# Kernel tuning notes

Hardware: AMD Instinct MI355X
Metric: run time of the kernel (lower is better)

Reference implementation:

```python
import jax, jax.numpy as jnp
import numpy as np

EPS_ATTN = 1e-5   # attention denominator eps (module eps)
EPS_LN = 1e-5     # nn.LayerNorm default eps


def _prime(x, proj):
    # Performer FAVOR+ hyperbolic positive features.
    # x: (B,H,L,dh), proj: (dh,m) -> (B,H,L,2m)
    dn = x.shape[-1] ** -0.25
    xn = dn * x
    d = jnp.einsum('bhld,dm->bhlm', xn, proj)
    diag = 0.5 * jnp.sum(xn * xn, axis=-1, keepdims=True)
    return jnp.concatenate([jnp.exp(d - diag), jnp.exp(-d - diag)], axis=-1)


def setup_inputs() -> dict:
    L, B, H, DH, DM, M = 2048, 4, 8, 64, 512, 256
    key = jax.random.key(0)
    k0, k1, k2 = jax.random.split(key, 3)
    h = jax.random.normal(k0, (L, B, DM), jnp.float32)
    w_qkv = jax.random.normal(k1, (H * 3 * DH, DM), jnp.float32) / np.sqrt(DM)
    w_o = jax.random.normal(k2, (DM, H * DH), jnp.float32) / np.sqrt(H * DH)
    ln_gamma = jnp.ones((DM,), jnp.float32)
    ln_beta = jnp.zeros((DM,), jnp.float32)
    # Gaussian orthogonal random matrix (blockwise QR), rows scaled by sqrt(dh)
    rng = np.random.default_rng(0)
    blocks = []
    for _ in range(M // DH):
        g = rng.standard_normal((DH, DH)).astype(np.float32)
        q, _ = np.linalg.qr(g)
        blocks.append(q.T)
    pm = np.concatenate(blocks, axis=0) * np.sqrt(DH)  # (M, DH)
    proj_matrix = jnp.asarray(pm.T.astype(np.float32))  # (DH, M)
    return {"h": h, "w_qkv": w_qkv, "w_o": w_o,
            "ln_gamma": ln_gamma, "ln_beta": ln_beta,
            "proj_matrix": proj_matrix}


def _forward(h, w_qkv, w_o, ln_gamma, ln_beta, proj_matrix):
    L, B, DM = h.shape
    DH, M = proj_matrix.shape
    H = w_qkv.shape[0] // (3 * DH)
    scale = DH ** -0.5

    qkv = (h @ w_qkv.T).reshape(L, B, H, 3 * DH)
    q, k, v = jnp.split(qkv, 3, axis=-1)
    q = jnp.transpose(q, (1, 2, 0, 3))  # (B,H,L,dh)
    k = jnp.transpose(k, (1, 2, 0, 3))
    v = jnp.transpose(v, (1, 2, 0, 3))

    qp = _prime(q, proj_matrix)  # (B,H,L,2M)
    kp = _prime(k, proj_matrix)
    kp = kp / jnp.sum(kp, axis=-1, keepdims=True)
    qp = qp / jnp.sum(qp, axis=-1, keepdims=True)

    den_acc = jnp.cumsum(kp, axis=2)
    denom = jnp.einsum('bhlm,bhlm->bhl', den_acc, qp)[..., None]  # (B,H,L,1)

    # fast_weight_sum: W_t = W_{t-1} + k_t v_t^T ; out_t = q_t @ W_t
    def step(W, xs):
        qt, kt, vt = xs  # (B,H,2M), (B,H,2M), (B,H,dh)
        W = W + kt[..., :, None] * vt[..., None, :]
        out = jnp.einsum('bhm,bhmd->bhd', qt, W)
        return W, out

    W0 = jnp.zeros((B, H, 2 * M, DH), h.dtype)
    xs = (jnp.transpose(qp, (2, 0, 1, 3)),
          jnp.transpose(kp, (2, 0, 1, 3)),
          jnp.transpose(v, (2, 0, 1, 3)))
    _, out = jax.lax.scan(step, W0, xs)  # (L,B,H,dh)
    out = jnp.transpose(out, (1, 2, 0, 3))  # (B,H,L,dh)

    out = scale * out / (denom + EPS_ATTN)
    out = jnp.transpose(out, (0, 2, 1, 3)).reshape(B, L, H * DH)  # (B,L,H*dh)
    out = jnp.swapaxes(out, 0, 1)  # (L,B,H*dh)

    attn_out = out @ w_o.T
    x = h + attn_out
    mu = jnp.mean(x, axis=-1, keepdims=True)
    var = jnp.mean((x - mu) ** 2, axis=-1, keepdims=True)
    return (x - mu) / jnp.sqrt(var + EPS_LN) * ln_gamma + ln_beta


def reference(h, w_qkv, w_o, ln_gamma, ln_beta, proj_matrix):
    return _forward(h, w_qkv, w_o, ln_gamma, ln_beta, proj_matrix)
```

## Files before the change

kernel.cpp:

```cpp
#include <hip/hip_runtime.h>
#include <hip/hip_fp16.h>
#include <math.h>

#define LSEQ 2048
#define NB 4
#define NH 8
#define DMID 512
#define CHK 128
#define SCALE 0.125f
#define DN 0.35355339059327373f
#define DN2 0.125f
#define LOG2E 1.4426950408889634f
#define EPS_ATTN 1e-5f
#define EPS_LN 1e-5f

typedef _Float16 f16x8 __attribute__((ext_vector_type(8)));
typedef _Float16 f16x4 __attribute__((ext_vector_type(4)));
typedef float f32x4 __attribute__((ext_vector_type(4)));

__device__ __forceinline__ float exp2a(float x) {
  float r;
  asm("v_exp_f32 %0, %1" : "=v"(r) : "v"(x));
  return r;
}

__device__ __forceinline__ void cvt16(const float* __restrict__ p,
                                      _Float16* __restrict__ dst) {
  float4 a = *(const float4*)p, b = *(const float4*)(p + 4);
  float4 c = *(const float4*)(p + 8), d = *(const float4*)(p + 12);
  f16x8 t0 = {(_Float16)a.x, (_Float16)a.y, (_Float16)a.z, (_Float16)a.w,
              (_Float16)b.x, (_Float16)b.y, (_Float16)b.z, (_Float16)b.w};
  f16x8 t1 = {(_Float16)c.x, (_Float16)c.y, (_Float16)c.z, (_Float16)c.w,
              (_Float16)d.x, (_Float16)d.y, (_Float16)d.z, (_Float16)d.w};
  *(f16x8*)dst = t0;
  *(f16x8*)(dst + 8) = t1;
}

__device__ __forceinline__ void cvt16r(const float4* __restrict__ r,
                                       _Float16* __restrict__ dst) {
  f16x8 t0 = {(_Float16)r[0].x, (_Float16)r[0].y, (_Float16)r[0].z,
              (_Float16)r[0].w, (_Float16)r[1].x, (_Float16)r[1].y,
              (_Float16)r[1].z, (_Float16)r[1].w};
  f16x8 t1 = {(_Float16)r[2].x, (_Float16)r[2].y, (_Float16)r[2].z,
              (_Float16)r[2].w, (_Float16)r[3].x, (_Float16)r[3].y,
              (_Float16)r[3].z, (_Float16)r[3].w};
  *(f16x8*)dst = t0;
  *(f16x8*)(dst + 8) = t1;
}

__device__ __forceinline__ void cvt8r(const float4* __restrict__ r,
                                      _Float16* __restrict__ dst) {
  f16x8 t0 = {(_Float16)r[0].x, (_Float16)r[0].y, (_Float16)r[0].z,
              (_Float16)r[0].w, (_Float16)r[1].x, (_Float16)r[1].y,
              (_Float16)r[1].z, (_Float16)r[1].w};
  *(f16x8*)dst = t0;
}

__global__ void k_diag(float* out, int n, float val) {
  int i = blockIdx.x * 256 + threadIdx.x;
  if (i < n) out[i] = val;
}

__global__ __launch_bounds__(256) void k_ptr(const float* __restrict__ proj,
                                             __half* __restrict__ projT) {
  int e = blockIdx.x * 256 + threadIdx.x;
  int n = e >> 6, k = e & 63;
  projT[e] = __float2half_rn(proj[k * 256 + n] * (DN * LOG2E));
}

__global__ __launch_bounds__(512) void k_qkv(
    const float* __restrict__ A, const float* __restrict__ Wq,
    __half* __restrict__ q, __half* __restrict__ k, __half* __restrict__ v) {
  __shared__ __align__(16) char smem[34816];
  _Float16* Ah = (_Float16*)smem;
  _Float16* Bh = (_Float16*)(smem + 20480);
  _Float16* Oh = (_Float16*)smem;

  const int tid = threadIdx.x;
  const int row0 = blockIdx.x * 256;
  const int col0 = blockIdx.y * 128;
  const int lane = tid & 63, wv = tid >> 6;
  const int ln15 = lane & 15, quad = lane >> 4;
  const int m0 = wv * 32;

  f32x4 Cacc[2][8];
  const f32x4 z4 = {0.f, 0.f, 0.f, 0.f};
#pragma unroll
  for (int mi = 0; mi < 2; ++mi)
#pragma unroll
    for (int nt = 0; nt < 8; ++nt) Cacc[mi][nt] = z4;

  const int sarow = tid >> 1, sac = (tid & 1) * 16;
  const float* aptr = A + (size_t)(row0 + sarow) * DMID + sac;
  const float* bptr = Wq + (size_t)(col0 + sarow) * DMID + sac;

  float4 ra[4], rb[4];
#pragma unroll
  for (int i = 0; i < 4; ++i) ra[i] = *(const float4*)(aptr + i * 4);
  if (tid < 256) {
#pragma unroll
    for (int i = 0; i < 4; ++i) rb[i] = *(const float4*)(bptr + i * 4);
  }

  for (int kt = 0; kt < DMID; kt += 32) {
    cvt16r(ra, &Ah[sarow * 40 + sac]);
    if (tid < 256) cvt16r(rb, &Bh[sarow * 40 + sac]);
    if (kt + 32 < DMID) {
#pragma unroll
      for (int i = 0; i < 4; ++i)
        ra[i] = *(const float4*)(aptr + kt + 32 + i * 4);
      if (tid < 256) {
#pragma unroll
        for (int i = 0; i < 4; ++i)
          rb[i] = *(const float4*)(bptr + kt + 32 + i * 4);
      }
    }
    asm volatile("s_waitcnt lgkmcnt(0)" ::: "memory");
    __builtin_amdgcn_s_barrier();
    asm volatile("" ::: "memory");

    f16x8 a0 = *(const f16x8*)&Ah[(m0 + ln15) * 40 + quad * 8];
    f16x8 a1 = *(const f16x8*)&Ah[(m0 + 16 + ln15) * 40 + quad * 8];
#pragma unroll
    for (int nt = 0; nt < 8; ++nt) {
      f16x8 bf = *(const f16x8*)&Bh[(nt * 16 + ln15) * 40 + quad * 8];
      Cacc[0][nt] = __builtin_amdgcn_mfma_f32_16x16x32_f16(a0, bf, Cacc[0][nt], 0, 0, 0);
      Cacc[1][nt] = __builtin_amdgcn_mfma_f32_16x16x32_f16(a1, bf, Cacc[1][nt], 0, 0, 0);
    }
    asm volatile("" ::: "memory");
    __builtin_amdgcn_s_barrier();
    asm volatile("" ::: "memory");
  }

  const int tr = tid >> 4, tc = tid & 15;
  const int col = col0 + tc * 8;
  const int hh = col / 192;
  const int rem = col - hh * 192;
  const int t = rem >> 6;
  const int d0 = rem & 63;
  __half* dstb = (t == 0) ? q : ((t == 1) ? k : v);

#pragma unroll
  for (int hf = 0; hf < 2; ++hf) {
    if ((wv >> 2) == hf) {
      int lm = (wv & 3) * 32;
#pragma unroll
      for (int mi = 0; mi < 2; ++mi)
#pragma unroll
        for (int nt = 0; nt < 8; ++nt)
#pragma unroll
          for (int r = 0; r < 4; ++r)
            Oh[(lm + mi * 16 + quad * 4 + r) * 136 + nt * 16 + ln15] =
                (_Float16)Cacc[mi][nt][r];
    }
    __syncthreads();
#pragma unroll
    for (int i = 0; i < 4; ++i) {
      int lrow = tr * 4 + i;
      int grow = row0 + hf * 128 + lrow;
      int l = grow >> 2, bb = grow & 3;
      f16x8 val = *(const f16x8*)&Oh[lrow * 136 + tc * 8];
      *(f16x8*)((_Float16*)dstb + (((size_t)(bb * NH + hh) * LSEQ + l) << 6) + d0) = val;
    }
    __syncthreads();
  }
}

__global__ __launch_bounds__(512) void k_dgemm(
    const __half* __restrict__ qsrc, const __half* __restrict__ ksrc,
    const __half* __restrict__ projT, __half* __restrict__ dqd,
    __half* __restrict__ dkd, float* __restrict__ nq,
    float* __restrict__ nk) {
  __shared__ __align__(16) char smem[37888];
  _Float16* Bt = (_Float16*)smem;
  float* g_l  = (float*)(smem + 36864);
  float* ps_l = (float*)(smem + 37376);
  _Float16* Oh = (_Float16*)smem;

  const int tid = threadIdx.x;
  const __half* src = blockIdx.y ? ksrc : qsrc;
  __half* dst = blockIdx.y ? dkd : dqd;
  float* nrm = blockIdx.y ? nk : nq;
  const size_t r0 = (size_t)blockIdx.x * 128;

  const int lane = tid & 63, wv = tid >> 6;
  const int ln15 = lane & 15, quad = lane >> 4;
  const int m0 = wv * 16;

#pragma unroll
  for (int it = 0; it < 4; ++it) {
    int e = it * 512 + tid;
    int n = e >> 3, seg = e & 7;
    *(f16x8*)&Bt[n * 72 + seg * 8] =
        *(const f16x8*)((const _Float16*)projT + n * 64 + seg * 8);
  }

  f16x8 afrag[2];
  float ss = 0.f;
  {
    const _Float16* rp = (const _Float16*)src + (r0 + m0 + ln15) * 64;
#pragma unroll
    for (int ks = 0; ks < 2; ++ks) {
      f16x8 x8 = *(const f16x8*)(rp + ks * 32 + quad * 8);
      afrag[ks] = x8;
#pragma unroll
      for (int j = 0; j < 8; ++j) {
        float xv = (float)x8[j];
        ss = fmaf(xv, xv, ss);
      }
    }
    ss += __shfl_xor(ss, 16);
    ss += __shfl_xor(ss, 32);
  }
  if (quad == 0) g_l[m0 + ln15] = 0.5f * DN2 * LOG2E * ss;
  __syncthreads();

  f32x4 Cacc[16];
  const f32x4 z4 = {0.f, 0.f, 0.f, 0.f};
#pragma unroll
  for (int nt = 0; nt < 16; ++nt) Cacc[nt] = z4;

#pragma unroll
  for (int ks = 0; ks < 2; ++ks) {
    f16x8 a0 = afrag[ks];
#pragma unroll
    for (int nt = 0; nt < 16; ++nt) {
      f16x8 bf = *(const f16x8*)&Bt[(nt * 16 + ln15) * 72 + ks * 32 + quad * 8];
      Cacc[nt] = __builtin_amdgcn_mfma_f32_16x16x32_f16(a0, bf, Cacc[nt], 0, 0, 0);
    }
  }

  float gv[4], pp[4];
#pragma unroll
  for (int r = 0; r < 4; ++r) {
    gv[r] = g_l[m0 + quad * 4 + r];
    pp[r] = 0.f;
  }
#pragma unroll
  for (int nt = 0; nt < 16; ++nt)
#pragma unroll
    for (int r = 0; r < 4; ++r) {
      float d = Cacc[nt][r];
      pp[r] += exp2a(d - gv[r]) + exp2a(-d - gv[r]);
    }
#pragma unroll
  for (int r = 0; r < 4; ++r) {
    float p = pp[r];
    p += __shfl_xor(p, 1); p += __shfl_xor(p, 2);
    p += __shfl_xor(p, 4); p += __shfl_xor(p, 8);
    if (ln15 == 0) ps_l[m0 + quad * 4 + r] = p;
  }

#pragma unroll
  for (int hf = 0; hf < 2; ++hf) {
    __syncthreads();
#pragma unroll
    for (int nt2 = 0; nt2 < 8; ++nt2) {
      int nt = hf * 8 + nt2;
#pragma unroll
      for (int r = 0; r < 4; ++r)
        Oh[(m0 + quad * 4 + r) * 136 + nt2 * 16 + ln15] =
            (_Float16)Cacc[nt][r];
    }
    __syncthreads();
#pragma unroll
    for (int it = 0; it < 4; ++it) {
      int e = it * 512 + tid;
      int row = e >> 4, seg = e & 15;
      *(f16x8*)((_Float16*)dst + (r0 + row) * 256 + hf * 128 + seg * 8) =
          *(const f16x8*)&Oh[row * 136 + seg * 8];
    }
  }
  if (tid < 128) nrm[r0 + tid] = g_l[tid] + __log2f(ps_l[tid]);
}

__global__ __launch_bounds__(512) void k_kv(
    const __half* __restrict__ dk, const float* __restrict__ nk,
    const __half* __restrict__ v, __half* __restrict__ KVt,
    float* __restrict__ Ks) {
  __shared__ __align__(16) char smem[52736];
  _Float16* kpT = (_Float16*)smem;
  _Float16* Vt  = (_Float16*)(smem + 34816);
  float* ck = (float*)(smem + 52224);
  _Float16* Oh2 = (_Float16*)smem;

  const int tid = threadIdx.x;
  const int cidx = blockIdx.x;
  const size_t rowbase = (size_t)cidx * CHK;
  const int lane = tid & 63, wv = tid >> 6;
  const int ln15 = lane & 15, quad = lane >> 4;

  if (tid < 128) ck[tid] = nk[rowbase + tid];
  {
    int s = tid & 127, dq0 = (tid >> 7) * 16;
    const _Float16* vsrc = (const _Float16*)v + (rowbase + s) * 64 + dq0;
    f16x8 v0 = ((const f16x8*)vsrc)[0];
    f16x8 v1 = ((const f16x8*)vsrc)[1];
#pragma unroll
    for (int j = 0; j < 8; ++j) {
      Vt[(dq0 + j) * 136 + s] = v0[j];
      Vt[(dq0 + 8 + j) * 136 + s] = v1[j];
    }
  }

  const int srow = tid >> 2;
  const int scol = (tid & 3) * 32;

  f16x8 bone;
#pragma unroll
  for (int j = 0; j < 8; ++j)
    bone[j] = (ln15 == 0) ? (_Float16)1.0f : (_Float16)0.0f;

  bool first = true;
#pragma unroll
  for (int cp = 0; cp < 2; ++cp) {
    f16x8 rk[4];
    const _Float16* dsrc =
        (const _Float16*)dk + (rowbase + srow) * 256 + cp * 128 + scol;
#pragma unroll
    for (int it = 0; it < 4; ++it) rk[it] = *(const f16x8*)(dsrc + it * 8);
    float c = ck[srow];
    if (first) { __syncthreads(); c = ck[srow]; }

#pragma unroll
    for (int sg = 0; sg < 2; ++sg) {
      const int i0 = sg * 256 + cp * 128;
      const float fsign = sg ? -1.f : 1.f;
      if (!first) __syncthreads();
      first = false;
#pragma unroll
      for (int it = 0; it < 4; ++it) {
        f16x8 d8 = rk[it];
#pragma unroll
        for (int j = 0; j < 8; ++j)
          kpT[(scol + it * 8 + j) * 136 + srow] =
              (_Float16)exp2a(fmaf((float)d8[j], fsign, -c));
      }
      __syncthreads();

      f32x4 Cacc[4], Kacc;
      const f32x4 z4 = {0.f, 0.f, 0.f, 0.f};
#pragma unroll
      for (int nt = 0; nt < 4; ++nt) Cacc[nt] = z4;
      Kacc = z4;
#pragma unroll
      for (int ks = 0; ks < 4; ++ks) {
        f16x8 a0 = *(const f16x8*)&kpT[(wv * 16 + ln15) * 136 + ks * 32 + quad * 8];
#pragma unroll
        for (int nt = 0; nt < 4; ++nt) {
          f16x8 bV = *(const f16x8*)&Vt[(nt * 16 + ln15) * 136 + ks * 32 + quad * 8];
          Cacc[nt] = __builtin_amdgcn_mfma_f32_16x16x32_f16(a0, bV, Cacc[nt], 0, 0, 0);
        }
        Kacc = __builtin_amdgcn_mfma_f32_16x16x32_f16(a0, bone, Kacc, 0, 0, 0);
      }
      if (ln15 == 0) {
#pragma unroll
        for (int r = 0; r < 4; ++r)
          Ks[(size_t)cidx * 512 + i0 + wv * 16 + quad * 4 + r] = Kacc[r];
      }
      __syncthreads();

#pragma unroll
      for (int nt = 0; nt < 4; ++nt) {
        f16x4 pack = {(_Float16)Cacc[nt][0], (_Float16)Cacc[nt][1],
                      (_Float16)Cacc[nt][2], (_Float16)Cacc[nt][3]};
        *(f16x4*)&Oh2[(nt * 16 + ln15) * 136 + wv * 16 + quad * 4] = pack;
      }
      __syncthreads();
      {
        int d = tid >> 3, part = tid & 7;
        _Float16* dstp =
            (_Float16*)KVt + (size_t)cidx * 32768 + d * 512 + i0 + part * 16;
        const _Float16* srcp = &Oh2[d * 136 + part * 16];
        *(f16x8*)(dstp) = *(const f16x8*)(srcp);
        *(f16x8*)(dstp + 8) = *(const f16x8*)(srcp + 8);
      }
    }
  }
}

__global__ __launch_bounds__(256) void k_scan(__half2* __restrict__ KV2,
                                              float* __restrict__ Ks) {
  const int bh = blockIdx.x;
  const int tid = threadIdx.x;
  if (blockIdx.y < 32) {
    uint2* p = (uint2*)(KV2 + (size_t)bh * 262144) + (blockIdx.y * 256 + tid);
    uint2 raw[16];
#pragma unroll
    for (int c = 0; c < 16; ++c) raw[c] = p[c * 8192];
    float ax0 = 0.f, ay0 = 0.f, ax1 = 0.f, ay1 = 0.f;
#pragma unroll
    for (int c = 0; c < 16; ++c) {
      __half2 h0 = *(__half2*)&raw[c].x;
      __half2 h1 = *(__half2*)&raw[c].y;
      float2 f0 = __half22float2(h0), f1 = __half22float2(h1);
      __half2 o0 = __floats2half2_rn(ax0, ay0);
      __half2 o1 = __floats2half2_rn(ax1, ay1);
      uint2 o;
      o.x = *(unsigned*)&o0;
      o.y = *(unsigned*)&o1;
      p[c * 8192] = o;
      ax0 += f0.x; ay0 += f0.y; ax1 += f1.x; ay1 += f1.y;
    }
  } else {
    int i = (blockIdx.y - 32) * 256 + tid;
    float* pk = Ks + (size_t)bh * 8192 + i;
    float vs[16];
#pragma unroll
    for (int c = 0; c < 16; ++c) vs[c] = pk[c * 512];
    float a = 0.f;
#pragma unroll
    for (int c = 0; c < 16; ++c) { pk[c * 512] = a; a += vs[c]; }
  }
}

__global__ __launch_bounds__(512) void k_attn(
    const __half* __restrict__ dq, const __half* __restrict__ dk,
    const float* __restrict__ nq, const float* __restrict__ nk,
    const __half* __restrict__ v, const __half* __restrict__ KVt,
    const float* __restrict__ Kpre, float* __restrict__ outb) {
  __shared__ __align__(16) char smem[53760];
  _Float16* qpT = (_Float16*)(smem);
  _Float16* kpT = (_Float16*)(smem + 18432);
  _Float16* WT  = (_Float16*)(smem + 36864);
  float*    KpT = (float*)(smem + 46080);
  float* cq_l   = (float*)(smem + 46336);
  float* ck_l   = (float*)(smem + 46848);
  _Float16* S_h = (_Float16*)(smem);
  _Float16* Vt  = (_Float16*)(smem + 34816);
  float* den1_l = (float*)(smem + 52224);
  float* den2_l = (float*)(smem + 52736);
  float* invd_l = (float*)(smem + 53248);

  const int tid = threadIdx.x;
  const int cidx = blockIdx.x;
  const int cc = cidx & 15, bh = cidx >> 4;
  const size_t rowb = (size_t)cidx * 128;
  const int lane = tid & 63;
  const int wv = tid >> 6;
  const int H = wv >> 2;
  const int m0 = (wv & 3) * 16;
  const int ln15 = lane & 15, quad = lane >> 4;

  if (tid < 128) cq_l[tid] = nq[rowb + tid];
  else if (tid < 256) ck_l[tid - 128] = nk[rowb + tid - 128];
  __syncthreads();

  const int c8 = tid & 7;
  const int r9 = tid >> 3;
  const int csrc = (c8 & 3) * 8;
  const float sgnf = (c8 < 4) ? 1.f : -1.f;

  const _Float16* qsrc = (const _Float16*)dq + (rowb + r9) * 256 + csrc;
  const _Float16* ksrc = (const _Float16*)dk + (rowb + r9) * 256 + csrc;
  const _Float16* wsrc = (const _Float16*)KVt + (size_t)cidx * 32768 +
                         r9 * 512 + ((c8 < 4) ? 0 : 256) + csrc;
  const float* kpsrc = Kpre + (size_t)cidx * 512 +
                       ((tid < 32) ? tid : (tid < 64 ? 224 + tid : 0));

  float cq[2], ck2[2];
#pragma unroll
  for (int p = 0; p < 2; ++p) {
    cq[p] = cq_l[r9 + p * 64];
    ck2[p] = ck_l[r9 + p * 64];
  }

  f16x8 rq[2], rk[2];
#pragma unroll
  for (int p = 0; p < 2; ++p) {
    rq[p] = *(const f16x8*)(qsrc + p * 16384);
    rk[p] = *(const f16x8*)(ksrc + p * 16384);
  }
  f16x8 wcur = *(const f16x8*)(wsrc);
  float kpcur = kpsrc[0];

  f32x4 Sacc[8], Oacc[4], Dacc;
  const f32x4 z4 = {0.f, 0.f, 0.f, 0.f};
#pragma unroll
  for (int nt = 0; nt < 8; ++nt) Sacc[nt] = z4;
#pragma unroll
  for (int nt = 0; nt < 4; ++nt) Oacc[nt] = z4;
  Dacc = z4;

  const int NSw = H ? 8 : 4;

  for (int it = 0; it < 8; ++it) {
    const int kb = it * 32;
    f16x8 wnxt;
    float kpnxt = 0.f;
    if (it < 7) {
      wnxt = *(const f16x8*)(wsrc + kb + 32);
      kpnxt = kpsrc[kb + 32];
    }

#pragma unroll
    for (int p = 0; p < 2; ++p) {
      f16x8 d = rq[p], t;
#pragma unroll
      for (int j = 0; j < 8; ++j)
        t[j] = (_Float16)exp2a(fmaf((float)d[j], sgnf, -cq[p]));
      *(f16x8*)&qpT[(r9 + p * 64) * 72 + c8 * 8] = t;
    }
#pragma unroll
    for (int p = 0; p < 2; ++p) {
      f16x8 d = rk[p], t;
#pragma unroll
      for (int j = 0; j < 8; ++j)
        t[j] = (_Float16)exp2a(fmaf((float)d[j], sgnf, -ck2[p]));
      *(f16x8*)&kpT[(r9 + p * 64) * 72 + c8 * 8] = t;
    }

    if (it < 7) {
#pragma unroll
      for (int p = 0; p < 2; ++p) {
        rq[p] = *(const f16x8*)(qsrc + p * 16384 + kb + 32);
        rk[p] = *(const f16x8*)(ksrc + p * 16384 + kb + 32);
      }
    }
    *(f16x8*)&WT[r9 * 72 + c8 * 8] = wcur;
    if (tid < 64) KpT[tid] = kpcur;

    asm volatile("s_waitcnt lgkmcnt(0)" ::: "memory");
    __builtin_amdgcn_s_barrier();
    asm volatile("" ::: "memory");

    __builtin_amdgcn_s_setprio(1);
#pragma unroll
    for (int ks = 0; ks < 2; ++ks) {
      f16x8 a0 = *(const f16x8*)&qpT[(H * 64 + m0 + ln15) * 72 + ks * 32 + quad * 8];
#pragma unroll
      for (int nt = 0; nt < 4; ++nt) {
        f16x8 bf = *(const f16x8*)&kpT[(nt * 16 + ln15) * 72 + ks * 32 + quad * 8];
        Sacc[nt] = __builtin_amdgcn_mfma_f32_16x16x32_f16(a0, bf, Sacc[nt], 0, 0, 0);
      }
      if (H) {
#pragma unroll
        for (int nt = 4; nt < 8; ++nt) {
          f16x8 bf = *(const f16x8*)&kpT[(nt * 16 + ln15) * 72 + ks * 32 + quad * 8];
          Sacc[nt] = __builtin_amdgcn_mfma_f32_16x16x32_f16(a0, bf, Sacc[nt], 0, 0, 0);
        }
      }
#pragma unroll
      for (int nt = 0; nt < 4; ++nt) {
        f16x8 bw = *(const f16x8*)&WT[(nt * 16 + ln15) * 72 + ks * 32 + quad * 8];
        Oacc[nt] = __builtin_amdgcn_mfma_f32_16x16x32_f16(a0, bw, Oacc[nt], 0, 0, 0);
      }
      f16x8 bk;
#pragma unroll
      for (int j = 0; j < 8; ++j)
        bk[j] = (ln15 == 0) ? (_Float16)KpT[ks * 32 + quad * 8 + j]
                            : (_Float16)0.f;
      Dacc = __builtin_amdgcn_mfma_f32_16x16x32_f16(a0, bk, Dacc, 0, 0, 0);
    }
    __builtin_amdgcn_s_setprio(0);

    asm volatile("" ::: "memory");
    __builtin_amdgcn_s_barrier();
    asm volatile("" ::: "memory");

    if (it < 7) { wcur = wnxt; kpcur = kpnxt; }
  }

  if (ln15 == 0) {
#pragma unroll
    for (int r = 0; r < 4; ++r)
      den2_l[H * 64 + m0 + quad * 4 + r] = Dacc[r];
  }
  {
    _Float16* S_me = S_h + H * 8704;
    float dp[4] = {0.f, 0.f, 0.f, 0.f};
#pragma unroll
    for (int nt = 0; nt < 8; ++nt) {
      if (nt < NSw) {
        int s = nt * 16 + ln15;
#pragma unroll
        for (int r = 0; r < 4; ++r) {
          int tl = m0 + quad * 4 + r;
          float vsv = (s <= H * 64 + tl) ? Sacc[nt][r] : 0.f;
          dp[r] += vsv;
          S_me[tl * 136 + s] = (_Float16)vsv;
        }
      }
    }
#pragma unroll
    for (int r = 0; r < 4; ++r) {
      float p = dp[r];
      p += __shfl_xor(p, 1); p += __shfl_xor(p, 2);
      p += __shfl_xor(p, 4); p += __shfl_xor(p, 8);
      if (ln15 == 0) den1_l[H * 64 + m0 + quad * 4 + r] = p;
    }
  }
  {
    int s = tid & 127, d0v = (tid >> 7) * 16;
    const _Float16* vsrc = (const _Float16*)v + (rowb + s) * 64 + d0v;
    f16x8 v0 = ((const f16x8*)vsrc)[0];
    f16x8 v1 = ((const f16x8*)vsrc)[1];
#pragma unroll
    for (int j = 0; j < 8; ++j) {
      Vt[(d0v + j) * 136 + s] = v0[j];
      Vt[(d0v + 8 + j) * 136 + s] = v1[j];
    }
  }
  __syncthreads();
  if (tid < 128)
    invd_l[tid] = SCALE / (den1_l[tid] + den2_l[tid] + EPS_ATTN);
  __syncthreads();
  {
    _Float16* S_me = S_h + H * 8704;
#pragma unroll
    for (int ks = 0; ks < 4; ++ks) {
      if (ks < (H ? 4 : 2)) {
        f16x8 aS0 = *(const f16x8*)&S_me[(m0 + ln15) * 136 + ks * 32 + quad * 8];
#pragma unroll
        for (int nt = 0; nt < 4; ++nt) {
          f16x8 bV = *(const f16x8*)&Vt[(nt * 16 + ln15) * 136 + ks * 32 + quad * 8];
          Oacc[nt] = __builtin_amdgcn_mfma_f32_16x16x32_f16(aS0, bV, Oacc[nt], 0, 0, 0);
        }
      }
    }
  }
  const int b = bh >> 3, hh = bh & 7;
  float ivv[4];
#pragma unroll
  for (int r = 0; r < 4; ++r)
    ivv[r] = invd_l[H * 64 + m0 + quad * 4 + r];
#pragma unroll
  for (int nt = 0; nt < 4; ++nt) {
    int dcol = nt * 16 + ln15;
#pragma unroll
    for (int r = 0; r < 4; ++r) {
      int l = cc * 128 + H * 64 + m0 + quad * 4 + r;
      outb[((size_t)l * 4 + b) * 512 + hh * 64 + dcol] = Oacc[nt][r] * ivv[r];
    }
  }
}

__global__ __launch_bounds__(256) void k_oproj(
    const float* __restrict__ A, const float* __restrict__ Wo,
    const float* __restrict__ hres, float* __restrict__ xout) {
  __shared__ __align__(16) char smem[17408];
  _Float16* Ah = (_Float16*)smem;
  _Float16* Bh = (_Float16*)(smem + 5120);
  _Float16* Oh = (_Float16*)smem;

  const int tid = threadIdx.x;
  const int row0 = blockIdx.x * 64;
  const int col0 = blockIdx.y * 128;
  const int lane = tid & 63, wv = tid >> 6;
  const int ln15 = lane & 15, quad = lane >> 4;
  const int m0 = wv * 16;

  f32x4 Cacc[8];
  const f32x4 z4 = {0.f, 0.f, 0.f, 0.f};
#pragma unroll
  for (int nt = 0; nt < 8; ++nt) Cacc[nt] = z4;

  const int arow = tid >> 2, asc = (tid & 3) * 8;
  const int brow = tid >> 1, bsc = (tid & 1) * 16;
  const float* aptr = A + (size_t)(row0 + arow) * DMID + asc;
  const float* bptr = Wo + (size_t)(col0 + brow) * DMID + bsc;

  float4 ra[2], rb[4];
#pragma unroll
  for (int i = 0; i < 2; ++i) ra[i] = *(const float4*)(aptr + i * 4);
#pragma unroll
  for (int i = 0; i < 4; ++i) rb[i] = *(const float4*)(bptr + i * 4);

  for (int kt = 0; kt < DMID; kt += 32) {
    cvt8r(ra, &Ah[arow * 40 + asc]);
    cvt16r(rb, &Bh[brow * 40 + bsc]);
    if (kt + 32 < DMID) {
#pragma unroll
      for (int i = 0; i < 2; ++i)
        ra[i] = *(const float4*)(aptr + kt + 32 + i * 4);
#pragma unroll
      for (int i = 0; i < 4; ++i)
        rb[i] = *(const float4*)(bptr + kt + 32 + i * 4);
    }
    asm volatile("s_waitcnt lgkmcnt(0)" ::: "memory");
    __builtin_amdgcn_s_barrier();
    asm volatile("" ::: "memory");

    f16x8 a0 = *(const f16x8*)&Ah[(m0 + ln15) * 40 + quad * 8];
#pragma unroll
    for (int nt = 0; nt < 8; ++nt) {
      f16x8 bf = *(const f16x8*)&Bh[(nt * 16 + ln15) * 40 + quad * 8];
      Cacc[nt] = __builtin_amdgcn_mfma_f32_16x16x32_f16(a0, bf, Cacc[nt], 0, 0, 0);
    }
    asm volatile("" ::: "memory");
    __builtin_amdgcn_s_barrier();
    asm volatile("" ::: "memory");
  }
#pragma unroll
  for (int nt = 0; nt < 8; ++nt)
#pragma unroll
    for (int r = 0; r < 4; ++r)
      Oh[(m0 + quad * 4 + r) * 136 + nt * 16 + ln15] = (_Float16)Cacc[nt][r];
  __syncthreads();
  const int tr = tid >> 4, tc = tid & 15;
#pragma unroll
  for (int i = 0; i < 4; ++i) {
    int lrow = tr * 4 + i;
    int grow = row0 + lrow;
    size_t base = (size_t)grow * 512 + col0 + tc * 8;
    f16x8 o = *(const f16x8*)&Oh[lrow * 136 + tc * 8];
    float4 h0 = *(const float4*)(hres + base);
    float4 h1 = *(const float4*)(hres + base + 4);
    *(float4*)(xout + base) =
        make_float4((float)o[0] + h0.x, (float)o[1] + h0.y,
                    (float)o[2] + h0.z, (float)o[3] + h0.w);
    *(float4*)(xout + base + 4) =
        make_float4((float)o[4] + h1.x, (float)o[5] + h1.y,
                    (float)o[6] + h1.z, (float)o[7] + h1.w);
  }
}

__global__ __launch_bounds__(256) void k_ln(float* __restrict__ x,
                                            const float* __restrict__ g,
                                            const float* __restrict__ bta) {
  __shared__ float ws_[4], wq_[4];
  const int row = blockIdx.x;
  const int tid = threadIdx.x;
  float2 vv = *(const float2*)(x + (size_t)row * 512 + tid * 2);
  float s = vv.x + vv.y;
  float sq = vv.x * vv.x + vv.y * vv.y;
#pragma unroll
  for (int off = 1; off < 64; off <<= 1) {
    s += __shfl_xor(s, off, 64);
    sq += __shfl_xor(sq, off, 64);
  }
  if ((tid & 63) == 0) { ws_[tid >> 6] = s; wq_[tid >> 6] = sq; }
  __syncthreads();
  s = ws_[0] + ws_[1] + ws_[2] + ws_[3];
  sq = wq_[0] + wq_[1] + wq_[2] + wq_[3];
  float mu = s * (1.f / 512.f);
  float var = sq * (1.f / 512.f) - mu * mu;
  float rstd = rsqrtf(var + EPS_LN);
  int c = tid * 2;
  float2 o;
  o.x = (vv.x - mu) * rstd * g[c] + bta[c];
  o.y = (vv.y - mu) * rstd * g[c + 1] + bta[c + 1];
  *(float2*)(x + (size_t)row * 512 + c) = o;
}

extern "C" void kernel_launch(void* const* d_in, const int* in_sizes, int n_in,
                              void* d_out, int out_size, void* d_ws,
                              size_t ws_size, hipStream_t stream) {
  const float* h    = (const float*)d_in[0];
  const float* wqkv = (const float*)d_in[1];
  const float* wo   = (const float*)d_in[2];
  const float* g    = (const float*)d_in[3];
  const float* bta  = (const float*)d_in[4];
  const float* proj = (const float*)d_in[5];
  float* out = (float*)d_out;
  char* wsb = (char*)d_ws;

  __half* q   = (__half*)(wsb + 0);
  __half* kb  = (__half*)(wsb + 8388608);
  __half* vb  = (__half*)(wsb + 16777216);
  __half* dq  = (__half*)(wsb + 25165824);
  __half* dk  = (__half*)(wsb + 58720256);
  float*  nq  = (float*)(wsb + 92274688);
  float*  nk  = (float*)(wsb + 92798976);
  __half* KVt = (__half*)(wsb + 93323264);
  float*  Ks  = (float*)(wsb + 126877696);
  __half* pT  = (__half*)(wsb + 127926272);
  float* outb = (float*)(wsb + 0);

  if (ws_size < 127959040ull) {
    float val = 1000.0f + (float)(ws_size >> 20);
    k_diag<<<(out_size + 255) / 256, 256, 0, stream>>>(out, out_size, val);
    return;
  }

  k_ptr  <<<dim3(64), 256, 0, stream>>>(proj, pT);
  k_qkv  <<<dim3(32, 12), 512, 0, stream>>>(h, wqkv, q, kb, vb);
  k_dgemm<<<dim3(512, 2), 512, 0, stream>>>(q, kb, pT, dq, dk, nq, nk);
  k_kv   <<<dim3(512), 512, 0, stream>>>(dk, nk, vb, KVt, Ks);
  k_scan <<<dim3(32, 34), 256, 0, stream>>>((__half2*)KVt, Ks);
  k_attn <<<dim3(512), 512, 0, stream>>>(dq, dk, nq, nk, vb, KVt, Ks, outb);
  k_oproj<<<dim3(128, 4), 256, 0, stream>>>(outb, wo, h, out);
  k_ln   <<<dim3(8192), 256, 0, stream>>>(out, g, bta);
}
```

Baseline: 223.4 us.

## Fuse output projection, residual add and LayerNorm into one kernel

Replaces the separate output-projection GEMM and LayerNorm kernels with one kernel in which each block computes 32 full rows of all 512 output columns. Residual add and LayerNorm statistics are then done in registers, with a shuffle plus shared-memory cross-wave reduction. This removes one launch and the extra write and read of the pre-norm activations. In exchange, each block now reloads the entire Wo matrix, and only 256 blocks are launched, which can lower parallelism and raise weight traffic.

```diff
diff --git a/kernel.cpp b/kernel.cpp
--- a/kernel.cpp
+++ b/kernel.cpp
@@ -46,14 +46,6 @@
               (_Float16)r[3].z, (_Float16)r[3].w};
   *(f16x8*)dst = t0;
   *(f16x8*)(dst + 8) = t1;
-}
-
-__device__ __forceinline__ void cvt8r(const float4* __restrict__ r,
-                                      _Float16* __restrict__ dst) {
-  f16x8 t0 = {(_Float16)r[0].x, (_Float16)r[0].y, (_Float16)r[0].z,
-              (_Float16)r[0].w, (_Float16)r[1].x, (_Float16)r[1].y,
-              (_Float16)r[1].z, (_Float16)r[1].w};
-  *(f16x8*)dst = t0;
 }
 
 __global__ void k_diag(float* out, int n, float val) {
@@ -635,112 +627,120 @@
   }
 }
 
-__global__ __launch_bounds__(256) void k_oproj(
+__global__ __launch_bounds__(512) void k_oproj_ln(
     const float* __restrict__ A, const float* __restrict__ Wo,
-    const float* __restrict__ hres, float* __restrict__ xout) {
-  __shared__ __align__(16) char smem[17408];
+    const float* __restrict__ hres, const float* __restrict__ g,
+    const float* __restrict__ bta, float* __restrict__ xout) {
+  __shared__ __align__(16) char smem[45568];
   _Float16* Ah = (_Float16*)smem;
-  _Float16* Bh = (_Float16*)(smem + 5120);
-  _Float16* Oh = (_Float16*)smem;
+  _Float16* Bh = (_Float16*)(smem + 2560);
+  float* s_l = (float*)(smem + 43520);
+  float* q_l = (float*)(smem + 44032);
 
   const int tid = threadIdx.x;
-  const int row0 = blockIdx.x * 64;
-  const int col0 = blockIdx.y * 128;
+  const int row0 = blockIdx.x * 32;
   const int lane = tid & 63, wv = tid >> 6;
   const int ln15 = lane & 15, quad = lane >> 4;
-  const int m0 = wv * 16;
+  const int mt = wv & 1;
+  const int nq4 = wv >> 1;
+  const int n0 = nq4 * 128;
 
   f32x4 Cacc[8];
   const f32x4 z4 = {0.f, 0.f, 0.f, 0.f};
 #pragma unroll
   for (int nt = 0; nt < 8; ++nt) Cacc[nt] = z4;
 
-  const int arow = tid >> 2, asc = (tid & 3) * 8;
-  const int brow = tid >> 1, bsc = (tid & 1) * 16;
-  const float* aptr = A + (size_t)(row0 + arow) * DMID + asc;
-  const float* bptr = Wo + (size_t)(col0 + brow) * DMID + bsc;
-
-  float4 ra[2], rb[4];
-#pragma unroll
-  for (int i = 0; i < 2; ++i) ra[i] = *(const float4*)(aptr + i * 4);
-#pragma unroll
-  for (int i = 0; i < 4; ++i) rb[i] = *(const float4*)(bptr + i * 4);
+  const int arow = tid >> 3, ac4 = (tid & 7) * 4;
+  const float* aptr = A + (size_t)(row0 + arow) * DMID + ac4;
+  const float* bptr = Wo + (size_t)tid * DMID;
+
+  float4 ra;
+  float4 rb[8];
+  if (tid < 256) ra = *(const float4*)(aptr);
+#pragma unroll
+  for (int i = 0; i < 8; ++i) rb[i] = *(const float4*)(bptr + i * 4);
 
   for (int kt = 0; kt < DMID; kt += 32) {
-    cvt8r(ra, &Ah[arow * 40 + asc]);
-    cvt16r(rb, &Bh[brow * 40 + bsc]);
+    if (tid < 256) {
+      _Float16* ad = &Ah[arow * 40 + ac4];
+      ad[0] = (_Float16)ra.x; ad[1] = (_Float16)ra.y;
+      ad[2] = (_Float16)ra.z; ad[3] = (_Float16)ra.w;
+    }
+    cvt16r(rb, &Bh[tid * 40]);
+    cvt16r(rb + 4, &Bh[tid * 40 + 16]);
     if (kt + 32 < DMID) {
-#pragma unroll
-      for (int i = 0; i < 2; ++i)
-        ra[i] = *(const float4*)(aptr + kt + 32 + i * 4);
-#pragma unroll
-      for (int i = 0; i < 4; ++i)
+      if (tid < 256) ra = *(const float4*)(aptr + kt + 32);
+#pragma unroll
+      for (int i = 0; i < 8; ++i)
         rb[i] = *(const float4*)(bptr + kt + 32 + i * 4);
     }
     asm volatile("s_waitcnt lgkmcnt(0)" ::: "memory");
     __builtin_amdgcn_s_barrier();
     asm volatile("" ::: "memory");
 
-    f16x8 a0 = *(const f16x8*)&Ah[(m0 + ln15) * 40 + quad * 8];
+    f16x8 a0 = *(const f16x8*)&Ah[(mt * 16 + ln15) * 40 + quad * 8];
 #pragma unroll
     for (int nt = 0; nt < 8; ++nt) {
-      f16x8 bf = *(const f16x8*)&Bh[(nt * 16 + ln15) * 40 + quad * 8];
+      f16x8 bf = *(const f16x8*)&Bh[(n0 + nt * 16 + ln15) * 40 + quad * 8];
       Cacc[nt] = __builtin_amdgcn_mfma_f32_16x16x32_f16(a0, bf, Cacc[nt], 0, 0, 0);
     }
     asm volatile("" ::: "memory");
     __builtin_amdgcn_s_barrier();
     asm volatile("" ::: "memory");
   }
-#pragma unroll
-  for (int nt = 0; nt < 8; ++nt)
-#pragma unroll
-    for (int r = 0; r < 4; ++r)
-      Oh[(m0 + quad * 4 + r) * 136 + nt * 16 + ln15] = (_Float16)Cacc[nt][r];
+
+  float xi[8][4];
+  float s[4] = {0.f, 0.f, 0.f, 0.f}, sq[4] = {0.f, 0.f, 0.f, 0.f};
+#pragma unroll
+  for (int nt = 0; nt < 8; ++nt) {
+    int col = n0 + nt * 16 + ln15;
+#pragma unroll
+    for (int r = 0; r < 4; ++r) {
+      int grow = row0 + mt * 16 + quad * 4 + r;
+      float x = Cacc[nt][r] + hres[(size_t)grow * 512 + col];
+      xi[nt][r] = x;
+      s[r] += x;
+      sq[r] = fmaf(x, x, sq[r]);
+    }
+  }
+#pragma unroll
+  for (int r = 0; r < 4; ++r) {
+    float a = s[r], b = sq[r];
+    a += __shfl_xor(a, 1); b += __shfl_xor(b, 1);
+    a += __shfl_xor(a, 2); b += __shfl_xor(b, 2);
+    a += __shfl_xor(a, 4); b += __shfl_xor(b, 4);
+    a += __shfl_xor(a, 8); b += __shfl_xor(b, 8);
+    if (ln15 == 0) {
+      int rloc = mt * 16 + quad * 4 + r;
+      s_l[rloc * 4 + nq4] = a;
+      q_l[rloc * 4 + nq4] = b;
+    }
+  }
   __syncthreads();
-  const int tr = tid >> 4, tc = tid & 15;
-#pragma unroll
-  for (int i = 0; i < 4; ++i) {
-    int lrow = tr * 4 + i;
-    int grow = row0 + lrow;
-    size_t base = (size_t)grow * 512 + col0 + tc * 8;
-    f16x8 o = *(const f16x8*)&Oh[lrow * 136 + tc * 8];
-    float4 h0 = *(const float4*)(hres + base);
-    float4 h1 = *(const float4*)(hres + base + 4);
-    *(float4*)(xout + base) =
-        make_float4((float)o[0] + h0.x, (float)o[1] + h0.y,
-                    (float)o[2] + h0.z, (float)o[3] + h0.w);
-    *(float4*)(xout + base + 4) =
-        make_float4((float)o[4] + h1.x, (float)o[5] + h1.y,
-                    (float)o[6] + h1.z, (float)o[7] + h1.w);
-  }
-}
-
-__global__ __launch_bounds__(256) void k_ln(float* __restrict__ x,
-                                            const float* __restrict__ g,
-                                            const float* __restrict__ bta) {
-  __shared__ float ws_[4], wq_[4];
-  const int row = blockIdx.x;
-  const int tid = threadIdx.x;
-  float2 vv = *(const float2*)(x + (size_t)row * 512 + tid * 2);
-  float s = vv.x + vv.y;
-  float sq = vv.x * vv.x + vv.y * vv.y;
-#pragma unroll
-  for (int off = 1; off < 64; off <<= 1) {
-    s += __shfl_xor(s, off, 64);
-    sq += __shfl_xor(sq, off, 64);
-  }
-  if ((tid & 63) == 0) { ws_[tid >> 6] = s; wq_[tid >> 6] = sq; }
-  __syncthreads();
-  s = ws_[0] + ws_[1] + ws_[2] + ws_[3];
-  sq = wq_[0] + wq_[1] + wq_[2] + wq_[3];
-  float mu = s * (1.f / 512.f);
-  float var = sq * (1.f / 512.f) - mu * mu;
-  float rstd = rsqrtf(var + EPS_LN);
-  int c = tid * 2;
-  float2 o;
-  o.x = (vv.x - mu) * rstd * g[c] + bta[c];
-  o.y = (vv.y - mu) * rstd * g[c + 1] + bta[c + 1];
-  *(float2*)(x + (size_t)row * 512 + c) = o;
+  float mu[4], rstd[4];
+#pragma unroll
+  for (int r = 0; r < 4; ++r) {
+    int rloc = mt * 16 + quad * 4 + r;
+    float a = s_l[rloc * 4] + s_l[rloc * 4 + 1] + s_l[rloc * 4 + 2] +
+              s_l[rloc * 4 + 3];
+    float b = q_l[rloc * 4] + q_l[rloc * 4 + 1] + q_l[rloc * 4 + 2] +
+              q_l[rloc * 4 + 3];
+    float m = a * (1.f / 512.f);
+    float var = b * (1.f / 512.f) - m * m;
+    mu[r] = m;
+    rstd[r] = rsqrtf(var + EPS_LN);
+  }
+#pragma unroll
+  for (int nt = 0; nt < 8; ++nt) {
+    int col = n0 + nt * 16 + ln15;
+    float gg = g[col], bb = bta[col];
+#pragma unroll
+    for (int r = 0; r < 4; ++r) {
+      int grow = row0 + mt * 16 + quad * 4 + r;
+      xout[(size_t)grow * 512 + col] =
+          (xi[nt][r] - mu[r]) * rstd[r] * gg + bb;
+    }
+  }
 }
 
 extern "C" void kernel_launch(void* const* d_in, const int* in_sizes, int n_in,
@@ -773,12 +773,11 @@
     return;
   }
 
-  k_ptr  <<<dim3(64), 256, 0, stream>>>(proj, pT);
-  k_qkv  <<<dim3(32, 12), 512, 0, stream>>>(h, wqkv, q, kb, vb);
-  k_dgemm<<<dim3(512, 2), 512, 0, stream>>>(q, kb, pT, dq, dk, nq, nk);
-  k_kv   <<<dim3(512), 512, 0, stream>>>(dk, nk, vb, KVt, Ks);
-  k_scan <<<dim3(32, 34), 256, 0, stream>>>((__half2*)KVt, Ks);
-  k_attn <<<dim3(512), 512, 0, stream>>>(dq, dk, nq, nk, vb, KVt, Ks, outb);
-  k_oproj<<<dim3(128, 4), 256, 0, stream>>>(outb, wo, h, out);
-  k_ln   <<<dim3(8192), 256, 0, stream>>>(out, g, bta);
-}
+  k_ptr     <<<dim3(64), 256, 0, stream>>>(proj, pT);
+  k_qkv     <<<dim3(32, 12), 512, 0, stream>>>(h, wqkv, q, kb, vb);
+  k_dgemm   <<<dim3(512, 2), 512, 0, stream>>>(q, kb, pT, dq, dk, nq, nk);
+  k_kv      <<<dim3(512), 512, 0, stream>>>(dk, nk, vb, KVt, Ks);
+  k_scan    <<<dim3(32, 34), 256, 0, stream>>>((__half2*)KVt, Ks);
+  k_attn    <<<dim3(512), 512, 0, stream>>>(dq, dk, nq, nk, vb, KVt, Ks, outb);
+  k_oproj_ln<<<dim3(256), 512, 0, stream>>>(outb, wo, h, g, bta, out);
+}
```

New measurement: 232.7 us. 4.1% more time.
